# Optimization experiments

Hardware: AMD Instinct MI355X
Metric: run time of the kernel (lower is better)

Reference implementation:

```python
import jax, jax.numpy as jnp
import numpy as np

NUM_HEADS = 16


def setup_inputs() -> dict:
    key = jax.random.key(0)
    k1, k2, k3 = jax.random.split(key, 3)
    b, d, s = 2, 1024, 2048
    x = jax.random.normal(k1, (b, d, s), dtype=jnp.float32)
    # torch nn.Linear(d, 3d) without bias == x @ W1 with W1 of shape (d, 3d)
    W1 = jax.random.normal(k2, (d, 3 * d), dtype=jnp.float32) * (d ** -0.5)
    W2 = jax.random.normal(k3, (d, d), dtype=jnp.float32) * (d ** -0.5)
    return {"x": x, "W1": W1, "W2": W2}


def reference(x, W1, W2):
    # x: (b, hidden_dim, s) -> (b, s, hidden_dim)
    b, d, s = x.shape
    h = NUM_HEADS
    hd = d // h
    xt = jnp.swapaxes(x, 1, 2)                       # (b, s, d)
    qkv = xt @ W1                                    # (b, s, 3d)
    qkv = qkv.reshape(b, s, 3, h, hd)
    qkv = jnp.transpose(qkv, (2, 0, 3, 1, 4))        # (3, b, h, s, hd)
    q, k, v = qkv[0], qkv[1], qkv[2]
    scale = hd ** -0.5
    scores = jnp.einsum("bhqd,bhkd->bhqk", q, k) * scale  # (b, h, s, s)
    # causal mask: same as torch code (adds float32 min where not lower-tri)
    neg = jnp.finfo(jnp.float32).min
    causal = jnp.tril(jnp.ones((s, s), dtype=bool))
    scores = jnp.where(causal[None, None, :, :], scores, scores + neg)
    attn = jax.nn.softmax(scores, axis=-1)           # dropout = identity (eval)
    out = jnp.einsum("bhqk,bhkd->bhqd", attn, v)     # (b, h, s, hd)
    out = jnp.transpose(out, (0, 2, 1, 3)).reshape(b, s, d)
    out = out @ W2                                   # (b, s, d)
    return jnp.swapaxes(out, 1, 2)                   # (b, d, s)
```

## Files before the change

### kernel.cpp

```cpp
#include <hip/hip_runtime.h>
#include <math.h>

#define B_  2
#define D_  1024
#define S_  2048
#define H_  16
#define HD_ 64
#define D3_ 3072
#define M_  4096

typedef __attribute__((ext_vector_type(8))) short short8;
typedef __attribute__((ext_vector_type(4))) float float4v;

__device__ __forceinline__ short f2bf(float f) {
    unsigned u = __builtin_bit_cast(unsigned, f);
    unsigned r = (u + 0x7FFFu + ((u >> 16) & 1u)) >> 16;
    return (short)r;
}

__device__ __forceinline__ unsigned cvt_pk_bf16(float lo, float hi) {
    unsigned r;
    asm("v_cvt_pk_bf16_f32 %0, %1, %2" : "=v"(r) : "v"(lo), "v"(hi));
    return r;
}

__device__ __forceinline__ float fast_exp2(float x) {
    float r;
    asm("v_exp_f32 %0, %1" : "=v"(r) : "v"(x));
    return r;
}

#define GLD16(gsrc, ldst)                                                      \
    __builtin_amdgcn_global_load_lds(                                          \
        (const __attribute__((address_space(1))) void*)(gsrc),                 \
        (__attribute__((address_space(3))) void*)(ldst), 16, 0, 0)

__global__ __launch_bounds__(256) void transpose_cvt_all(const float* __restrict__ x,
                                                         short* __restrict__ xt,
                                                         const float* __restrict__ W1,
                                                         short* __restrict__ W1t,
                                                         const float* __restrict__ W2,
                                                         short* __restrict__ W2t) {
    __shared__ short t[64][66];
    const int bid = (int)blockIdx.x;
    const float* in;
    short* out;
    int C, R, rb, cb;
    if (bid < 1024) {
        const int z = bid >> 9, tt = bid & 511;
        R = D_; C = S_;
        cb = tt & 31; rb = tt >> 5;
        in = x + (size_t)z * D_ * S_;
        out = xt + (size_t)z * D_ * S_;
    } else if (bid < 1792) {
        const int tt = bid - 1024;
        R = D_; C = D3_;
        cb = tt % 48; rb = tt / 48;
        in = W1; out = W1t;
    } else {
        const int tt = bid - 1792;
        R = D_; C = D_;
        cb = tt & 15; rb = tt >> 4;
        in = W2; out = W2t;
    }
    const int r0 = rb * 64, c0 = cb * 64;
    const int tx = threadIdx.x & 31, ty = threadIdx.x >> 5;
    #pragma unroll
    for (int i = ty; i < 64; i += 8) {
        const float2 v = *(const float2*)&in[(size_t)(r0 + i) * C + c0 + tx * 2];
        t[i][tx * 2]     = f2bf(v.x);
        t[i][tx * 2 + 1] = f2bf(v.y);
    }
    __syncthreads();
    #pragma unroll
    for (int j = ty; j < 64; j += 8) {
        short2 v;
        v.x = t[tx * 2][j];
        v.y = t[tx * 2 + 1][j];
        *(short2*)&out[(size_t)(c0 + j) * R + r0 + tx * 2] = v;
    }
}

__device__ __forceinline__ void gemm_core(const short* __restrict__ A,
                                          const short* __restrict__ Bt,
                                          int m0, int n0,
                                          short* As, short* Bs,
                                          float4v acc[4][4]) {
    const int tid = threadIdx.x;
    const int lane = tid & 63, w = tid >> 6;
    const int wr = (w >> 1) * 64, wc = (w & 1) * 64;
    const int srow = lane >> 2;
    const int scol = ((lane & 3) ^ ((srow >> 1) & 3)) * 8;
    const int rr = lane & 15;
    const int kc = ((lane >> 4) ^ ((rr >> 1) & 3)) * 8;
    for (int k0 = 0; k0 < 1024; k0 += 32) {
        #pragma unroll
        for (int j = 0; j < 2; ++j) {
            const int ch = 2 * w + j;
            GLD16(A  + (size_t)(m0 + ch * 16 + srow) * 1024 + k0 + scol,
                  As + ch * 512 + lane * 8);
            GLD16(Bt + (size_t)(n0 + ch * 16 + srow) * 1024 + k0 + scol,
                  Bs + ch * 512 + lane * 8);
        }
        __syncthreads();
        short8 a[4], b[4];
        #pragma unroll
        for (int m = 0; m < 4; ++m)
            a[m] = *(const short8*)&As[(wr + m * 16 + rr) * 32 + kc];
        #pragma unroll
        for (int n = 0; n < 4; ++n)
            b[n] = *(const short8*)&Bs[(wc + n * 16 + rr) * 32 + kc];
        #pragma unroll
        for (int m = 0; m < 4; ++m)
            #pragma unroll
            for (int n = 0; n < 4; ++n)
                acc[m][n] = __builtin_amdgcn_mfma_f32_16x16x32_bf16(a[m], b[n], acc[m][n], 0, 0, 0);
        __syncthreads();
    }
}

__global__ __launch_bounds__(256) void gemm_qkv_mfma(const short* __restrict__ xt,
                                                     const short* __restrict__ W1t,
                                                     short* __restrict__ q,
                                                     short* __restrict__ kk,
                                                     short* __restrict__ vt) {
    __shared__ short As[128 * 32], Bs[128 * 32];
    float4v acc[4][4];
    #pragma unroll
    for (int m = 0; m < 4; ++m)
        #pragma unroll
        for (int n = 0; n < 4; ++n) acc[m][n] = (float4v){0.f, 0.f, 0.f, 0.f};
    const int bid = (int)blockIdx.x;
    const int xcd = bid & 7, r = bid >> 3;
    const int mt = (xcd & 3) * 8 + (r & 7);
    const int nt = (xcd >> 2) * 12 + (r >> 3);
    const int m0 = mt * 128, n0 = nt * 128;
    gemm_core(xt, W1t, m0, n0, As, Bs, acc);
    const int lane = threadIdx.x & 63, w = threadIdx.x >> 6;
    const int wr = (w >> 1) * 64, wc = (w & 1) * 64;
    const float qscale = 0.125f * 1.44269504f;
    #pragma unroll
    for (int n = 0; n < 4; ++n) {
        const int gcol = n0 + wc + n * 16 + (lane & 15);
        const int which = gcol >> 10, hh = (gcol >> 6) & 15, hd = gcol & 63;
        #pragma unroll
        for (int m = 0; m < 4; ++m) {
            #pragma unroll
            for (int ri = 0; ri < 4; ++ri) {
                const int grow = m0 + wr + m * 16 + (lane >> 4) * 4 + ri;
                const int bb = grow >> 11, ss = grow & (S_ - 1);
                float av = acc[m][n][ri];
                if (which == 0) av *= qscale;
                const short v = f2bf(av);
                if (which == 0)      q [((size_t)(bb * H_ + hh) * S_ + ss) * HD_ + hd] = v;
                else if (which == 1) kk[((size_t)(bb * H_ + hh) * S_ + ss) * HD_ + hd] = v;
                else                 vt[((size_t)(bb * H_ + hh) * HD_ + hd) * S_ + ss] = v;
            }
        }
    }
}

__global__ __launch_bounds__(256) void attn_mfma(const short* __restrict__ q,
                                                 const short* __restrict__ k,
                                                 const short* __restrict__ vt,
                                                 short* __restrict__ ao) {
    __shared__ short Ks[2][64 * 64];
    __shared__ short Vts[2][64 * 64];
    __shared__ short Ps[64 * 64];
    __shared__ float sums[64];
    const int tid = threadIdx.x;
    const int lane = tid & 63, w = tid >> 6;
    const int bid = (int)blockIdx.x;
    const int xcd = bid & 7, slot = bid >> 3;
    const int bh = xcd * 4 + (slot & 3);
    const int qpair = slot >> 2;
    const size_t base = (size_t)bh * S_ * HD_;
    const short* qp = q + base;
    const short* kp = k + base;
    const short* vp = vt + base;
    const int bb = bh >> 4, hh = bh & 15;
    const int wrow = w * 16;

    for (int half = 0; half < 2; ++half) {
        const int qt = (half == 0) ? qpair : 31 - qpair;
        const int q0 = qt * 64;
        short8 qf[2];
        #pragma unroll
        for (int ks = 0; ks < 2; ++ks)
            qf[ks] = *(const short8*)&qp[(size_t)(q0 + wrow + (lane & 15)) * HD_
                                         + ks * 32 + (lane >> 4) * 8];
        float4v accO[4];
        float lsum = 0.f;
        #pragma unroll
        for (int n = 0; n < 4; ++n) accO[n] = (float4v){0.f, 0.f, 0.f, 0.f};

        const int nkb = qt + 1;
        __syncthreads();
        #pragma unroll
        for (int j = 0; j < 2; ++j) {
            const int g = (w * 2 + j) * 64 + lane;
            const int r = g >> 3, cs = g & 7;
            const int co = (cs ^ (r & 7)) << 3;
            GLD16(kp + (size_t)r * HD_ + co, &Ks[0][g * 8]);
            GLD16(vp + (size_t)r * S_ + co,  &Vts[0][g * 8]);
        }
        int cur = 0;
        for (int kb = 0; kb < nkb; ++kb) {
            const int kv0 = kb * 64;
            __syncthreads();
            if (kb + 1 < nkb) {
                const int kv1 = kv0 + 64;
                #pragma unroll
                for (int j = 0; j < 2; ++j) {
                    const int g = (w * 2 + j) * 64 + lane;
                    const int r = g >> 3, cs = g & 7;
                    const int co = (cs ^ (r & 7)) << 3;
                    GLD16(kp + (size_t)(kv1 + r) * HD_ + co, &Ks[cur ^ 1][g * 8]);
                    GLD16(vp + (size_t)r * S_ + kv1 + co,    &Vts[cur ^ 1][g * 8]);
                }
            }
            float4v accS[4];
            #pragma unroll
            for (int n = 0; n < 4; ++n) accS[n] = (float4v){0.f, 0.f, 0.f, 0.f};
            #pragma unroll
            for (int ks = 0; ks < 2; ++ks) {
                #pragma unroll
                for (int n = 0; n < 4; ++n) {
                    const int rowk = n * 16 + (lane & 15);
                    const int ch = ks * 4 + (lane >> 4);
                    const short8 kf = *(const short8*)&Ks[cur][rowk * 64 + ((ch ^ (rowk & 7)) << 3)];
                    accS[n] = __builtin_amdgcn_mfma_f32_16x16x32_bf16(kf, qf[ks], accS[n], 0, 0, 0);
                }
            }
            const bool diag = (kb == qt);
            const int qg = q0 + wrow + (lane & 15);
            const int prow = wrow + (lane & 15);
            #pragma unroll
            for (int n = 0; n < 4; ++n) {
                const int kvb = kv0 + n * 16 + ((lane >> 4) << 2);
                float p[4];
                if (diag) {
                    const int dlim = qg - kvb;
                    #pragma unroll
                    for (int ri = 0; ri < 4; ++ri)
                        p[ri] = (ri <= dlim) ? fast_exp2(accS[n][ri]) : 0.f;
                } else {
                    #pragma unroll
                    for (int ri = 0; ri < 4; ++ri)
                        p[ri] = fast_exp2(accS[n][ri]);
                }
                lsum += (p[0] + p[1]) + (p[2] + p[3]);
                const unsigned lo = cvt_pk_bf16(p[0], p[1]);
                const unsigned hi = cvt_pk_bf16(p[2], p[3]);
                const int col = n * 16 + ((lane >> 4) << 2);
                const int ch = col >> 3;
                const int addr = prow * 64 + ((ch ^ (prow & 7)) << 3) + (col & 7);
                *(uint2*)&Ps[addr] = (uint2){lo, hi};
            }
            #pragma unroll
            for (int ks = 0; ks < 2; ++ks) {
                const int prow2 = wrow + (lane & 15);
                const int chp = ks * 4 + (lane >> 4);
                const short8 pf = *(const short8*)&Ps[prow2 * 64 + ((chp ^ (prow2 & 7)) << 3)];
                #pragma unroll
                for (int n = 0; n < 4; ++n) {
                    const int vrow = n * 16 + (lane & 15);
                    const int ch = ks * 4 + (lane >> 4);
                    const short8 vf = *(const short8*)&Vts[cur][vrow * 64 + ((ch ^ (vrow & 7)) << 3)];
                    accO[n] = __builtin_amdgcn_mfma_f32_16x16x32_bf16(pf, vf, accO[n], 0, 0, 0);
                }
            }
            cur ^= 1;
        }
        {
            float t = lsum;
            t += __shfl_xor(t, 16);
            t += __shfl_xor(t, 32);
            if (lane < 16) sums[wrow + lane] = t;
        }
        #pragma unroll
        for (int ri = 0; ri < 4; ++ri) {
            const int lrow = wrow + ((lane >> 4) << 2) + ri;
            const float inv = 1.f / sums[lrow];
            const int grow = q0 + lrow;
            #pragma unroll
            for (int n = 0; n < 4; ++n) {
                const int col = hh * 64 + n * 16 + (lane & 15);
                ao[((size_t)(bb * S_ + grow)) * D_ + col] = f2bf(accO[n][ri] * inv);
            }
        }
    }
}

__global__ __launch_bounds__(256) void gemm_out_mfma(const short* __restrict__ W2t,
                                                     const short* __restrict__ ao,
                                                     float* __restrict__ out) {
    __shared__ short As[128 * 32], Bs[128 * 32];
    float4v acc[4][4];
    #pragma unroll
    for (int m = 0; m < 4; ++m)
        #pragma unroll
        for (int n = 0; n < 4; ++n) acc[m][n] = (float4v){0.f, 0.f, 0.f, 0.f};
    const int m0 = blockIdx.y * 128, n0 = blockIdx.x * 128;
    gemm_core(W2t, ao, m0, n0, As, Bs, acc);
    const int lane = threadIdx.x & 63, w = threadIdx.x >> 6;
    const int wr = (w >> 1) * 64, wc = (w & 1) * 64;
    #pragma unroll
    for (int m = 0; m < 4; ++m) {
        #pragma unroll
        for (int ri = 0; ri < 4; ++ri) {
            const int grow = m0 + wr + m * 16 + (lane >> 4) * 4 + ri;
            #pragma unroll
            for (int n = 0; n < 4; ++n) {
                const int gcol = n0 + wc + n * 16 + (lane & 15);
                const int bb = gcol >> 11, ss = gcol & (S_ - 1);
                out[(size_t)bb * D_ * S_ + (size_t)grow * S_ + ss] = acc[m][n][ri];
            }
        }
    }
}

extern "C" void kernel_launch(void* const* d_in, const int* in_sizes, int n_in,
                              void* d_out, int out_size, void* d_ws, size_t ws_size,
                              hipStream_t stream) {
    const float* x  = (const float*)d_in[0];
    const float* W1 = (const float*)d_in[1];
    const float* W2 = (const float*)d_in[2];
    float* out = (float*)d_out;

    short* xt  = (short*)d_ws;
    short* W1t = xt  + (size_t)M_ * D_;
    short* W2t = W1t + (size_t)D3_ * D_;
    short* q   = W2t + (size_t)D_ * D_;
    short* kk  = q   + (size_t)B_ * H_ * S_ * HD_;
    short* vt  = kk  + (size_t)B_ * H_ * S_ * HD_;
    short* ao  = vt  + (size_t)B_ * H_ * S_ * HD_;

    transpose_cvt_all<<<dim3(2048), 256, 0, stream>>>(x, xt, W1, W1t, W2, W2t);
    gemm_qkv_mfma<<<dim3(768), 256, 0, stream>>>(xt, W1t, q, kk, vt);
    attn_mfma<<<dim3(512), 256, 0, stream>>>(q, kk, vt, ao);
    gemm_out_mfma<<<dim3(M_ / 128, D_ / 128), 256, 0, stream>>>(W2t, ao, out);
}
```

Baseline: 114.3 us.

## Double-buffer GEMM LDS tiles, add MFMA priority hints, XCD-aware out-proj tiling

The shared GEMM core now uses two LDS buffers so global loads for the next K slice are issued while MFMAs run on the current one. This hides load latency at the cost of twice the LDS per block. The attention kernel raises wave priority around its MFMA sections with s_setprio. The output projection switches to a 1D grid with an XCD-aware tile mapping, meant to improve L2 reuse of W2 and ao tiles per chiplet.

```diff
diff --git a/kernel.cpp b/kernel.cpp
--- a/kernel.cpp
+++ b/kernel.cpp
@@ -81,41 +81,60 @@
     }
 }
 
+__device__ __forceinline__ void gemm_stage(const short* __restrict__ A,
+                                           const short* __restrict__ Bt,
+                                           int m0, int n0, int k0,
+                                           short* As, short* Bs,
+                                           int w, int lane) {
+    const int srow = lane >> 2;
+    const int scol = ((lane & 3) ^ ((srow >> 1) & 3)) * 8;
+    #pragma unroll
+    for (int j = 0; j < 2; ++j) {
+        const int ch = 2 * w + j;
+        GLD16(A  + (size_t)(m0 + ch * 16 + srow) * 1024 + k0 + scol,
+              As + ch * 512 + lane * 8);
+        GLD16(Bt + (size_t)(n0 + ch * 16 + srow) * 1024 + k0 + scol,
+              Bs + ch * 512 + lane * 8);
+    }
+}
+
+__device__ __forceinline__ void gemm_compute(const short* As, const short* Bs,
+                                             float4v acc[4][4],
+                                             int lane, int wr, int wc) {
+    const int rr = lane & 15;
+    const int kc = ((lane >> 4) ^ ((rr >> 1) & 3)) * 8;
+    short8 a[4], b[4];
+    #pragma unroll
+    for (int m = 0; m < 4; ++m)
+        a[m] = *(const short8*)&As[(wr + m * 16 + rr) * 32 + kc];
+    #pragma unroll
+    for (int n = 0; n < 4; ++n)
+        b[n] = *(const short8*)&Bs[(wc + n * 16 + rr) * 32 + kc];
+    #pragma unroll
+    for (int m = 0; m < 4; ++m)
+        #pragma unroll
+        for (int n = 0; n < 4; ++n)
+            acc[m][n] = __builtin_amdgcn_mfma_f32_16x16x32_bf16(a[m], b[n], acc[m][n], 0, 0, 0);
+}
+
 __device__ __forceinline__ void gemm_core(const short* __restrict__ A,
                                           const short* __restrict__ Bt,
                                           int m0, int n0,
-                                          short* As, short* Bs,
+                                          short* As0, short* Bs0,
+                                          short* As1, short* Bs1,
                                           float4v acc[4][4]) {
     const int tid = threadIdx.x;
     const int lane = tid & 63, w = tid >> 6;
     const int wr = (w >> 1) * 64, wc = (w & 1) * 64;
-    const int srow = lane >> 2;
-    const int scol = ((lane & 3) ^ ((srow >> 1) & 3)) * 8;
-    const int rr = lane & 15;
-    const int kc = ((lane >> 4) ^ ((rr >> 1) & 3)) * 8;
-    for (int k0 = 0; k0 < 1024; k0 += 32) {
-        #pragma unroll
-        for (int j = 0; j < 2; ++j) {
-            const int ch = 2 * w + j;
-            GLD16(A  + (size_t)(m0 + ch * 16 + srow) * 1024 + k0 + scol,
-                  As + ch * 512 + lane * 8);
-            GLD16(Bt + (size_t)(n0 + ch * 16 + srow) * 1024 + k0 + scol,
-                  Bs + ch * 512 + lane * 8);
-        }
+    gemm_stage(A, Bt, m0, n0, 0, As0, Bs0, w, lane);
+    for (int t = 0; t < 32; t += 2) {
         __syncthreads();
-        short8 a[4], b[4];
-        #pragma unroll
-        for (int m = 0; m < 4; ++m)
-            a[m] = *(const short8*)&As[(wr + m * 16 + rr) * 32 + kc];
-        #pragma unroll
-        for (int n = 0; n < 4; ++n)
-            b[n] = *(const short8*)&Bs[(wc + n * 16 + rr) * 32 + kc];
-        #pragma unroll
-        for (int m = 0; m < 4; ++m)
-            #pragma unroll
-            for (int n = 0; n < 4; ++n)
-                acc[m][n] = __builtin_amdgcn_mfma_f32_16x16x32_bf16(a[m], b[n], acc[m][n], 0, 0, 0);
+        gemm_stage(A, Bt, m0, n0, (t + 1) * 32, As1, Bs1, w, lane);
+        gemm_compute(As0, Bs0, acc, lane, wr, wc);
         __syncthreads();
+        if (t + 2 < 32)
+            gemm_stage(A, Bt, m0, n0, (t + 2) * 32, As0, Bs0, w, lane);
+        gemm_compute(As1, Bs1, acc, lane, wr, wc);
     }
 }
 
@@ -124,7 +143,7 @@
                                                      short* __restrict__ q,
                                                      short* __restrict__ kk,
                                                      short* __restrict__ vt) {
-    __shared__ short As[128 * 32], Bs[128 * 32];
+    __shared__ short As[2][128 * 32], Bs[2][128 * 32];
     float4v acc[4][4];
     #pragma unroll
     for (int m = 0; m < 4; ++m)
@@ -135,7 +154,7 @@
     const int mt = (xcd & 3) * 8 + (r & 7);
     const int nt = (xcd >> 2) * 12 + (r >> 3);
     const int m0 = mt * 128, n0 = nt * 128;
-    gemm_core(xt, W1t, m0, n0, As, Bs, acc);
+    gemm_core(xt, W1t, m0, n0, As[0], Bs[0], As[1], Bs[1], acc);
     const int lane = threadIdx.x & 63, w = threadIdx.x >> 6;
     const int wr = (w >> 1) * 64, wc = (w & 1) * 64;
     const float qscale = 0.125f * 1.44269504f;
@@ -222,6 +241,7 @@
             float4v accS[4];
             #pragma unroll
             for (int n = 0; n < 4; ++n) accS[n] = (float4v){0.f, 0.f, 0.f, 0.f};
+            __builtin_amdgcn_s_setprio(1);
             #pragma unroll
             for (int ks = 0; ks < 2; ++ks) {
                 #pragma unroll
@@ -232,6 +252,7 @@
                     accS[n] = __builtin_amdgcn_mfma_f32_16x16x32_bf16(kf, qf[ks], accS[n], 0, 0, 0);
                 }
             }
+            __builtin_amdgcn_s_setprio(0);
             const bool diag = (kb == qt);
             const int qg = q0 + wrow + (lane & 15);
             const int prow = wrow + (lane & 15);
@@ -257,6 +278,7 @@
                 const int addr = prow * 64 + ((ch ^ (prow & 7)) << 3) + (col & 7);
                 *(uint2*)&Ps[addr] = (uint2){lo, hi};
             }
+            __builtin_amdgcn_s_setprio(1);
             #pragma unroll
             for (int ks = 0; ks < 2; ++ks) {
                 const int prow2 = wrow + (lane & 15);
@@ -270,6 +292,7 @@
                     accO[n] = __builtin_amdgcn_mfma_f32_16x16x32_bf16(pf, vf, accO[n], 0, 0, 0);
                 }
             }
+            __builtin_amdgcn_s_setprio(0);
             cur ^= 1;
         }
         {
@@ -295,14 +318,18 @@
 __global__ __launch_bounds__(256) void gemm_out_mfma(const short* __restrict__ W2t,
                                                      const short* __restrict__ ao,
                                                      float* __restrict__ out) {
-    __shared__ short As[128 * 32], Bs[128 * 32];
+    __shared__ short As[2][128 * 32], Bs[2][128 * 32];
     float4v acc[4][4];
     #pragma unroll
     for (int m = 0; m < 4; ++m)
         #pragma unroll
         for (int n = 0; n < 4; ++n) acc[m][n] = (float4v){0.f, 0.f, 0.f, 0.f};
-    const int m0 = blockIdx.y * 128, n0 = blockIdx.x * 128;
-    gemm_core(W2t, ao, m0, n0, As, Bs, acc);
+    const int bid = (int)blockIdx.x;
+    const int xcd = bid & 7, r = bid >> 3;
+    const int mt = (xcd & 1) * 4 + (r & 3);
+    const int nt = (xcd >> 1) * 8 + (r >> 2);
+    const int m0 = mt * 128, n0 = nt * 128;
+    gemm_core(W2t, ao, m0, n0, As[0], Bs[0], As[1], Bs[1], acc);
     const int lane = threadIdx.x & 63, w = threadIdx.x >> 6;
     const int wr = (w >> 1) * 64, wc = (w & 1) * 64;
     #pragma unroll
@@ -339,5 +366,5 @@
     transpose_cvt_all<<<dim3(2048), 256, 0, stream>>>(x, xt, W1, W1t, W2, W2t);
     gemm_qkv_mfma<<<dim3(768), 256, 0, stream>>>(xt, W1t, q, kk, vt);
     attn_mfma<<<dim3(512), 256, 0, stream>>>(q, kk, vt, ao);
-    gemm_out_mfma<<<dim3(M_ / 128, D_ / 128), 256, 0, stream>>>(W2t, ao, out);
-}
+    gemm_out_mfma<<<dim3(256), 256, 0, stream>>>(W2t, ao, out);
+}
```

New measurement: 118.2 us. +3.4%, slower.
